# Optimization experiments

Measured on AMD Instinct MI355X. Metric: run time of the kernel, lower is better.

## Reference

```python
import jax, jax.numpy as jnp
import numpy as np

B, N, K = 16, 4096, 32

def setup_inputs() -> dict:
    key = jax.random.key(0)
    k0, k1, k2, k3, k4, k5 = jax.random.split(key, 6)
    frames_rot = jax.random.normal(k0, (B, N, 3, 3), jnp.float32)
    frames_trans = jax.random.normal(k1, (B, N, 3), jnp.float32)
    pair_rot = jax.random.normal(k2, (B, N, K, 3, 3), jnp.float32)
    pair_trans = jax.random.normal(k3, (B, N, K, 3), jnp.float32)
    confidences = jax.random.uniform(k4, (B, N, K, 1), jnp.float32)
    topology = jax.random.randint(k5, (B, N, K), 0, N, jnp.int32)
    return {"frames_rot": frames_rot, "frames_trans": frames_trans,
            "pair_rot": pair_rot, "pair_trans": pair_trans,
            "confidences": confidences, "topology": topology}


def _proj_with_svd(m):
    """Kabsch projection of batched [..., 3, 3] matrices onto SO(3) (det=+1)."""
    u, s, vh = jnp.linalg.svd(m, full_matrices=False)
    V = jnp.swapaxes(vh, -1, -2)
    d = jnp.sign(jnp.linalg.det(jnp.matmul(V, jnp.swapaxes(u, -1, -2))))  # [...]
    d3 = jnp.concatenate([jnp.ones(d.shape + (2,), m.dtype), d[..., None]], axis=-1)  # diag(1,1,d)
    # rot = V @ diag(1,1,d) @ u^T
    return jnp.einsum('...ik,...k,...jk->...ij', V, d3, u)


def reference(frames_rot, frames_trans, pair_rot, pair_trans, confidences, topology):
    # gather neighbor frames T_j: [B,N,K,3,3] / [B,N,K,3]
    gather = jax.vmap(lambda f, t: f[t])
    Tj_rot = gather(frames_rot, topology)
    Tj_trans = gather(frames_trans, topology)

    # normalized confidences p_ij over neighbors K
    w = jnp.squeeze(confidences, axis=-1)             # [B,N,K]
    p = w / jnp.sum(w, axis=2, keepdims=True)         # [B,N,K]

    # compose rigids: T_j * T_ji
    comp_rot = jnp.einsum('bnkij,bnkjl->bnkil', Tj_rot, pair_rot)                 # [B,N,K,3,3]
    comp_trans = jnp.einsum('bnkij,bnkj->bnki', Tj_rot, pair_trans) + Tj_trans    # [B,N,K,3]

    # confidence-weighted average over neighbors
    avg_rot = jnp.einsum('bnk,bnkij->bnij', p, comp_rot)    # [B,N,3,3]
    avg_trans = jnp.einsum('bnk,bnki->bni', p, comp_trans)  # [B,N,3]

    # project averaged rot onto SO(3), then invert (transpose) as in the module
    rot = _proj_with_svd(avg_rot)
    rot_inv = jnp.swapaxes(rot, -1, -2)                     # invert_rots of a rotation

    # pack (rot 9 + trans 3) -> [B,N,12]
    return jnp.concatenate([rot_inv.reshape(B, N, 9), avg_trans], axis=-1)
```

## Files before the change

kernel.cpp:

```cpp
#include <hip/hip_runtime.h>
#include <math.h>

#define N_RES 4096
#define KNB 32
#define BN_TOTAL 65536

typedef float v4f __attribute__((ext_vector_type(4)));
typedef int v4i __attribute__((ext_vector_type(4)));

template <int p, int q>
__device__ __forceinline__ void jacobi_rot(float S[3][3], float V[3][3]) {
    float apq = S[p][q];
    if (fabsf(apq) > 1e-20f) {
        float app = S[p][p], aqq = S[q][q];
        float tau = (aqq - app) / (2.0f * apq);
        float tt = (tau >= 0.0f ? 1.0f : -1.0f) / (fabsf(tau) + sqrtf(1.0f + tau * tau));
        float c = 1.0f / sqrtf(1.0f + tt * tt);
        float s = tt * c;
#pragma unroll
        for (int i = 0; i < 3; i++) {
            float Sip = S[i][p], Siq = S[i][q];
            S[i][p] = c * Sip - s * Siq;
            S[i][q] = s * Sip + c * Siq;
        }
#pragma unroll
        for (int i = 0; i < 3; i++) {
            float Spi = S[p][i], Sqi = S[q][i];
            S[p][i] = c * Spi - s * Sqi;
            S[q][i] = s * Spi + c * Sqi;
        }
#pragma unroll
        for (int i = 0; i < 3; i++) {
            float Vip = V[i][p], Viq = V[i][q];
            V[i][p] = c * Vip - s * Viq;
            V[i][q] = s * Vip + c * Viq;
        }
    }
}

template <int A, int Bc>
__device__ __forceinline__ void sort_pair(float lam[3], float V[3][3]) {
    if (lam[A] < lam[Bc]) {
        float tl = lam[A]; lam[A] = lam[Bc]; lam[Bc] = tl;
#pragma unroll
        for (int i = 0; i < 3; i++) {
            float tv = V[i][A]; V[i][A] = V[i][Bc]; V[i][Bc] = tv;
        }
    }
}

__device__ __forceinline__ void project_and_store(const float M[3][3],
                                                  float t0, float t1, float t2,
                                                  float* outp) {
    float S[3][3];
#pragma unroll
    for (int i = 0; i < 3; i++)
#pragma unroll
        for (int j = 0; j < 3; j++)
            S[i][j] = M[0][i] * M[0][j] + M[1][i] * M[1][j] + M[2][i] * M[2][j];
    float V[3][3] = {{1, 0, 0}, {0, 1, 0}, {0, 0, 1}};

#pragma unroll
    for (int sweep = 0; sweep < 4; sweep++) {
        jacobi_rot<0, 1>(S, V);
        jacobi_rot<0, 2>(S, V);
        jacobi_rot<1, 2>(S, V);
    }

    float lam[3] = {S[0][0], S[1][1], S[2][2]};
    sort_pair<0, 1>(lam, V);
    sort_pair<1, 2>(lam, V);
    sort_pair<0, 1>(lam, V);

    float detV = V[0][0] * (V[1][1] * V[2][2] - V[1][2] * V[2][1]) -
                 V[0][1] * (V[1][0] * V[2][2] - V[1][2] * V[2][0]) +
                 V[0][2] * (V[1][0] * V[2][1] - V[1][1] * V[2][0]);
    if (detV < 0.0f) { V[0][2] = -V[0][2]; V[1][2] = -V[1][2]; V[2][2] = -V[2][2]; }

    float Bm[3][3];
#pragma unroll
    for (int i = 0; i < 3; i++)
#pragma unroll
        for (int j = 0; j < 3; j++)
            Bm[i][j] = M[i][0] * V[0][j] + M[i][1] * V[1][j] + M[i][2] * V[2][j];

    float u0[3] = {Bm[0][0], Bm[1][0], Bm[2][0]};
    float n0 = u0[0] * u0[0] + u0[1] * u0[1] + u0[2] * u0[2];
    float rn0 = 1.0f / sqrtf(fmaxf(n0, 1e-24f));
    u0[0] *= rn0; u0[1] *= rn0; u0[2] *= rn0;

    float b1[3] = {Bm[0][1], Bm[1][1], Bm[2][1]};
    float d01 = u0[0] * b1[0] + u0[1] * b1[1] + u0[2] * b1[2];
    float u1[3] = {b1[0] - d01 * u0[0], b1[1] - d01 * u0[1], b1[2] - d01 * u0[2]};
    float n1 = u1[0] * u1[0] + u1[1] * u1[1] + u1[2] * u1[2];
    float rn1 = 1.0f / sqrtf(fmaxf(n1, 1e-24f));
    u1[0] *= rn1; u1[1] *= rn1; u1[2] *= rn1;

    float u2[3] = {u0[1] * u1[2] - u0[2] * u1[1],
                   u0[2] * u1[0] - u0[0] * u1[2],
                   u0[0] * u1[1] - u0[1] * u1[0]};

    float R[9];
#pragma unroll
    for (int i = 0; i < 3; i++) {
        float Ui0 = (i == 0 ? u0[0] : (i == 1 ? u0[1] : u0[2]));
        float Ui1 = (i == 0 ? u1[0] : (i == 1 ? u1[1] : u1[2]));
        float Ui2 = (i == 0 ? u2[0] : (i == 1 ? u2[1] : u2[2]));
#pragma unroll
        for (int j = 0; j < 3; j++)
            R[i * 3 + j] = Ui0 * V[j][0] + Ui1 * V[j][1] + Ui2 * V[j][2];
    }

    v4f* o4 = (v4f*)outp;
    o4[0] = (v4f){R[0], R[1], R[2], R[3]};
    o4[1] = (v4f){R[4], R[5], R[6], R[7]};
    o4[2] = (v4f){R[8], t0, t1, t2};
}

__global__ __launch_bounds__(256) void repack_kernel(
    const float* __restrict__ frames_rot,
    const float* __restrict__ frames_trans,
    float* __restrict__ pk)
{
    int row = blockIdx.x * 256 + threadIdx.x;
    const float* fr = frames_rot + (size_t)row * 9;
    const float* ft = frames_trans + (size_t)row * 3;
    v4f a = {fr[0], fr[1], fr[2], fr[3]};
    v4f b = {fr[4], fr[5], fr[6], fr[7]};
    v4f c = {fr[8], ft[0], ft[1], ft[2]};
    v4f* o = (v4f*)(pk + (size_t)row * 16);
    o[0] = a; o[1] = b; o[2] = c;
}

__global__ __launch_bounds__(256) void accum_kernel(
    const float* __restrict__ pk,
    const float* __restrict__ pair_rot,
    const float* __restrict__ pair_trans,
    const float* __restrict__ conf,
    const int* __restrict__ topo,
    float* __restrict__ acc)
{
    int tid = threadIdx.x;
    int bid = blockIdx.x;

    int xcd = bid & 7;
    int slot = bid >> 3;
    int batch = xcd + ((slot >> 7) << 3);
    int chunk = slot & 127;

    int elem = batch * N_RES + chunk * 32 + (tid >> 3);
    int t = tid & 7;

    size_t kbase = (size_t)elem * KNB + (size_t)t * 4;
    const v4f* pr4 = (const v4f*)(pair_rot + kbase * 9);
    const v4f* pt4 = (const v4f*)(pair_trans + kbase * 3);
    const v4f* cf4 = (const v4f*)(conf + kbase);
    const v4i* tp4 = (const v4i*)(topo + kbase);

    float prl[36];
#pragma unroll
    for (int i = 0; i < 9; i++) {
        v4f v = __builtin_nontemporal_load(pr4 + i);
        prl[4 * i + 0] = v.x; prl[4 * i + 1] = v.y;
        prl[4 * i + 2] = v.z; prl[4 * i + 3] = v.w;
    }
    float ptl[12];
#pragma unroll
    for (int i = 0; i < 3; i++) {
        v4f v = __builtin_nontemporal_load(pt4 + i);
        ptl[4 * i + 0] = v.x; ptl[4 * i + 1] = v.y;
        ptl[4 * i + 2] = v.z; ptl[4 * i + 3] = v.w;
    }
    v4f wv = __builtin_nontemporal_load(cf4);
    float wl[4] = {wv.x, wv.y, wv.z, wv.w};
    v4i jv = __builtin_nontemporal_load(tp4);
    int jl[4] = {jv.x, jv.y, jv.z, jv.w};

    float Macc[9] = {0, 0, 0, 0, 0, 0, 0, 0, 0};
    float tacc[3] = {0, 0, 0};
    float wsum = 0.0f;

    size_t pkbase = (size_t)batch * N_RES * 16;

#pragma unroll
    for (int kk = 0; kk < 4; kk++) {
        int j = jl[kk];
        const v4f* row = (const v4f*)(pk + pkbase + (size_t)j * 16);
        v4f fa = row[0], fb = row[1], fc = row[2];
        float r[9] = {fa.x, fa.y, fa.z, fa.w, fb.x, fb.y, fb.z, fb.w, fc.x};
        float tj[3] = {fc.y, fc.z, fc.w};

        float w = wl[kk];
        const float* pr = prl + kk * 9;
        const float* pt = ptl + kk * 3;
#pragma unroll
        for (int i = 0; i < 3; i++) {
#pragma unroll
            for (int l = 0; l < 3; l++) {
                float cij = r[i * 3 + 0] * pr[0 * 3 + l] +
                            r[i * 3 + 1] * pr[1 * 3 + l] +
                            r[i * 3 + 2] * pr[2 * 3 + l];
                Macc[i * 3 + l] += w * cij;
            }
            float ct = r[i * 3 + 0] * pt[0] + r[i * 3 + 1] * pt[1] +
                       r[i * 3 + 2] * pt[2] + tj[i];
            tacc[i] += w * ct;
        }
        wsum += w;
    }

#pragma unroll
    for (int st = 1; st <= 4; st <<= 1) {
#pragma unroll
        for (int i = 0; i < 9; i++) Macc[i] += __shfl_xor(Macc[i], st);
#pragma unroll
        for (int i = 0; i < 3; i++) tacc[i] += __shfl_xor(tacc[i], st);
        wsum += __shfl_xor(wsum, st);
    }

    if (t == 0) {
        v4f* o = (v4f*)(acc + (size_t)elem * 16);
        o[0] = (v4f){Macc[0], Macc[1], Macc[2], Macc[3]};
        o[1] = (v4f){Macc[4], Macc[5], Macc[6], Macc[7]};
        o[2] = (v4f){Macc[8], tacc[0], tacc[1], tacc[2]};
        o[3] = (v4f){wsum, 0.0f, 0.0f, 0.0f};
    }
}

__global__ __launch_bounds__(256) void solve_kernel(
    const float* __restrict__ acc,
    float* __restrict__ out)
{
    int elem = blockIdx.x * 256 + threadIdx.x;
    const v4f* a4 = (const v4f*)(acc + (size_t)elem * 16);
    v4f A0 = a4[0], A1 = a4[1], A2 = a4[2], A3 = a4[3];
    float inv_w = 1.0f / fmaxf(A3.x, 1e-20f);
    float M[3][3] = {{A0.x * inv_w, A0.y * inv_w, A0.z * inv_w},
                     {A0.w * inv_w, A1.x * inv_w, A1.y * inv_w},
                     {A1.z * inv_w, A1.w * inv_w, A2.x * inv_w}};
    float t0 = A2.y * inv_w, t1 = A2.z * inv_w, t2 = A2.w * inv_w;
    project_and_store(M, t0, t1, t2, out + (size_t)elem * 12);
}

__global__ __launch_bounds__(256) void fused_kernel(
    const float* __restrict__ frames_rot, const float* __restrict__ frames_trans,
    const float* __restrict__ pair_rot, const float* __restrict__ pair_trans,
    const float* __restrict__ conf, const int* __restrict__ topo,
    float* __restrict__ out)
{
    int tid = threadIdx.x;
    int bid = blockIdx.x;
    int xcd = bid & 7;
    int slot = bid >> 3;
    int batch = xcd + ((slot >> 7) << 3);
    int chunk = slot & 127;
    int elem = batch * N_RES + chunk * 32 + (tid >> 3);
    int t = tid & 7;

    const float* fr_b = frames_rot + (size_t)batch * N_RES * 9;
    const float* ft_b = frames_trans + (size_t)batch * N_RES * 3;

    size_t kbase = (size_t)elem * KNB + (size_t)t * 4;
    const v4f* pr4 = (const v4f*)(pair_rot + kbase * 9);
    const v4f* pt4 = (const v4f*)(pair_trans + kbase * 3);
    const v4f* cf4 = (const v4f*)(conf + kbase);
    const v4i* tp4 = (const v4i*)(topo + kbase);

    float prl[36];
#pragma unroll
    for (int i = 0; i < 9; i++) {
        v4f v = __builtin_nontemporal_load(pr4 + i);
        prl[4 * i] = v.x; prl[4 * i + 1] = v.y; prl[4 * i + 2] = v.z; prl[4 * i + 3] = v.w;
    }
    float ptl[12];
#pragma unroll
    for (int i = 0; i < 3; i++) {
        v4f v = __builtin_nontemporal_load(pt4 + i);
        ptl[4 * i] = v.x; ptl[4 * i + 1] = v.y; ptl[4 * i + 2] = v.z; ptl[4 * i + 3] = v.w;
    }
    v4f wv = __builtin_nontemporal_load(cf4);
    float wl[4] = {wv.x, wv.y, wv.z, wv.w};
    v4i jv = __builtin_nontemporal_load(tp4);
    int jl[4] = {jv.x, jv.y, jv.z, jv.w};

    float Macc[9] = {0, 0, 0, 0, 0, 0, 0, 0, 0};
    float tacc[3] = {0, 0, 0};
    float wsum = 0.0f;

#pragma unroll
    for (int kk = 0; kk < 4; kk++) {
        int j = jl[kk];
        const float* Rj = fr_b + j * 9;
        const float* Tj = ft_b + j * 3;
        float r[9];
#pragma unroll
        for (int i = 0; i < 9; i++) r[i] = Rj[i];
        float tj[3];
#pragma unroll
        for (int i = 0; i < 3; i++) tj[i] = Tj[i];
        float w = wl[kk];
        const float* pr = prl + kk * 9;
        const float* pt = ptl + kk * 3;
#pragma unroll
        for (int i = 0; i < 3; i++) {
#pragma unroll
            for (int l = 0; l < 3; l++) {
                float cij = r[i * 3] * pr[l] + r[i * 3 + 1] * pr[3 + l] + r[i * 3 + 2] * pr[6 + l];
                Macc[i * 3 + l] += w * cij;
            }
            float ct = r[i * 3] * pt[0] + r[i * 3 + 1] * pt[1] + r[i * 3 + 2] * pt[2] + tj[i];
            tacc[i] += w * ct;
        }
        wsum += w;
    }

#pragma unroll
    for (int st = 1; st <= 4; st <<= 1) {
#pragma unroll
        for (int i = 0; i < 9; i++) Macc[i] += __shfl_xor(Macc[i], st);
#pragma unroll
        for (int i = 0; i < 3; i++) tacc[i] += __shfl_xor(tacc[i], st);
        wsum += __shfl_xor(wsum, st);
    }

    float inv_w = 1.0f / fmaxf(wsum, 1e-20f);
    float M[3][3];
#pragma unroll
    for (int i = 0; i < 3; i++)
#pragma unroll
        for (int j = 0; j < 3; j++) M[i][j] = Macc[i * 3 + j] * inv_w;

    if (t == 0)
        project_and_store(M, tacc[0] * inv_w, tacc[1] * inv_w, tacc[2] * inv_w,
                          out + (size_t)elem * 12);
}

extern "C" void kernel_launch(void* const* d_in, const int* in_sizes, int n_in,
                              void* d_out, int out_size, void* d_ws, size_t ws_size,
                              hipStream_t stream) {
    const float* frames_rot = (const float*)d_in[0];
    const float* frames_trans = (const float*)d_in[1];
    const float* pair_rot = (const float*)d_in[2];
    const float* pair_trans = (const float*)d_in[3];
    const float* conf = (const float*)d_in[4];
    const int* topo = (const int*)d_in[5];
    float* out = (float*)d_out;

    const size_t PK_BYTES = (size_t)BN_TOTAL * 16 * sizeof(float);
    const size_t need = 2 * PK_BYTES;

    if (ws_size >= need) {
        float* pk = (float*)d_ws;
        float* acc = pk + (size_t)BN_TOTAL * 16;
        hipLaunchKernelGGL(repack_kernel, dim3(BN_TOTAL / 256), dim3(256), 0, stream,
                           frames_rot, frames_trans, pk);
        hipLaunchKernelGGL(accum_kernel, dim3(BN_TOTAL * 8 / 256), dim3(256), 0, stream,
                           pk, pair_rot, pair_trans, conf, topo, acc);
        hipLaunchKernelGGL(solve_kernel, dim3(BN_TOTAL / 256), dim3(256), 0, stream,
                           acc, out);
    } else {
        hipLaunchKernelGGL(fused_kernel, dim3(BN_TOTAL * 8 / 256), dim3(256), 0, stream,
                           frames_rot, frames_trans, pair_rot, pair_trans, conf, topo, out);
    }
}
```

Measured before the change: 202.5 us.

## Stage pair rotations through LDS and interleave neighbor assignment for coalescing

The accumulation kernel now stages each block's pair_rot data in shared memory in two halves using contiguous 16-byte loads spread across all threads. Threads then read their neighbors' rotations from LDS, and neighbors are assigned with stride 8 so that conf, topo and pair_trans loads coalesce across lanes. Gathers of neighbor frames are software-pipelined (two rows prefetched ahead), and occupancy is hinted with launch_bounds(256,8). This adds __syncthreads barriers and scalar loads for pair_trans, but aims to cut scattered per-thread 144-byte streaming reads.

```diff
diff --git a/kernel.cpp b/kernel.cpp
--- a/kernel.cpp
+++ b/kernel.cpp
@@ -132,7 +132,9 @@
     o[0] = a; o[1] = b; o[2] = c;
 }
 
-__global__ __launch_bounds__(256) void accum_kernel(
+#define LDS_E_STRIDE 148
+
+__global__ __launch_bounds__(256, 8) void accum_kernel(
     const float* __restrict__ pk,
     const float* __restrict__ pair_rot,
     const float* __restrict__ pair_trans,
@@ -140,73 +142,96 @@
     const int* __restrict__ topo,
     float* __restrict__ acc)
 {
+    __shared__ float lds_rot[32 * LDS_E_STRIDE];
+
     int tid = threadIdx.x;
     int bid = blockIdx.x;
 
     int xcd = bid & 7;
     int slot = bid >> 3;
     int batch = xcd + ((slot >> 7) << 3);
-    int chunk = slot & 127;
-
-    int elem = batch * N_RES + chunk * 32 + (tid >> 3);
+    int chunkidx = slot & 127;
+    int elem0 = batch * N_RES + chunkidx * 32;
+
+    int e = tid >> 3;
     int t = tid & 7;
-
-    size_t kbase = (size_t)elem * KNB + (size_t)t * 4;
-    const v4f* pr4 = (const v4f*)(pair_rot + kbase * 9);
-    const v4f* pt4 = (const v4f*)(pair_trans + kbase * 3);
-    const v4f* cf4 = (const v4f*)(conf + kbase);
-    const v4i* tp4 = (const v4i*)(topo + kbase);
-
-    float prl[36];
-#pragma unroll
-    for (int i = 0; i < 9; i++) {
-        v4f v = __builtin_nontemporal_load(pr4 + i);
-        prl[4 * i + 0] = v.x; prl[4 * i + 1] = v.y;
-        prl[4 * i + 2] = v.z; prl[4 * i + 3] = v.w;
-    }
+    int elem_g = elem0 + e;
+
+    float wl[4];
+    int jl[4];
     float ptl[12];
 #pragma unroll
-    for (int i = 0; i < 3; i++) {
-        v4f v = __builtin_nontemporal_load(pt4 + i);
-        ptl[4 * i + 0] = v.x; ptl[4 * i + 1] = v.y;
-        ptl[4 * i + 2] = v.z; ptl[4 * i + 3] = v.w;
-    }
-    v4f wv = __builtin_nontemporal_load(cf4);
-    float wl[4] = {wv.x, wv.y, wv.z, wv.w};
-    v4i jv = __builtin_nontemporal_load(tp4);
-    int jl[4] = {jv.x, jv.y, jv.z, jv.w};
+    for (int s = 0; s < 4; s++) {
+        size_t nidx = (size_t)elem_g * KNB + t + 8 * s;
+        wl[s] = __builtin_nontemporal_load(conf + nidx);
+        jl[s] = __builtin_nontemporal_load(topo + nidx);
+#pragma unroll
+        for (int c = 0; c < 3; c++)
+            ptl[s * 3 + c] = __builtin_nontemporal_load(pair_trans + nidx * 3 + c);
+    }
+
+    const float* pkb = pk + (size_t)batch * N_RES * 16;
+    v4f g0a, g0b, g0c, g1a, g1b, g1c;
+    {
+        const v4f* r0 = (const v4f*)(pkb + (size_t)jl[0] * 16);
+        const v4f* r1 = (const v4f*)(pkb + (size_t)jl[1] * 16);
+        g0a = r0[0]; g0b = r0[1]; g0c = r0[2];
+        g1a = r1[0]; g1b = r1[1]; g1c = r1[2];
+    }
 
     float Macc[9] = {0, 0, 0, 0, 0, 0, 0, 0, 0};
     float tacc[3] = {0, 0, 0};
-    float wsum = 0.0f;
-
-    size_t pkbase = (size_t)batch * N_RES * 16;
-
-#pragma unroll
-    for (int kk = 0; kk < 4; kk++) {
-        int j = jl[kk];
-        const v4f* row = (const v4f*)(pk + pkbase + (size_t)j * 16);
-        v4f fa = row[0], fb = row[1], fc = row[2];
-        float r[9] = {fa.x, fa.y, fa.z, fa.w, fb.x, fb.y, fb.z, fb.w, fc.x};
-        float tj[3] = {fc.y, fc.z, fc.w};
-
-        float w = wl[kk];
-        const float* pr = prl + kk * 9;
-        const float* pt = ptl + kk * 3;
-#pragma unroll
-        for (int i = 0; i < 3; i++) {
-#pragma unroll
-            for (int l = 0; l < 3; l++) {
-                float cij = r[i * 3 + 0] * pr[0 * 3 + l] +
-                            r[i * 3 + 1] * pr[1 * 3 + l] +
-                            r[i * 3 + 2] * pr[2 * 3 + l];
-                Macc[i * 3 + l] += w * cij;
+    float wsum = wl[0] + wl[1] + wl[2] + wl[3];
+
+#pragma unroll
+    for (int ch = 0; ch < 2; ch++) {
+        for (int i = tid; i < 1152; i += 256) {
+            int se = i / 36;
+            int r = i - se * 36;
+            const v4f* gp = (const v4f*)(pair_rot +
+                ((size_t)(elem0 + se) * KNB + ch * 16) * 9) + r;
+            v4f v = __builtin_nontemporal_load(gp);
+            *(v4f*)(lds_rot + se * LDS_E_STRIDE + r * 4) = v;
+        }
+        __syncthreads();
+
+#pragma unroll
+        for (int sc = 0; sc < 2; sc++) {
+            int s = 2 * ch + sc;
+            float w = wl[s];
+            const float* lp = lds_rot + e * LDS_E_STRIDE + 9 * (t + 8 * sc);
+            float pr[9];
+#pragma unroll
+            for (int c = 0; c < 9; c++) pr[c] = lp[c];
+
+            v4f fa = (s & 1) ? g1a : g0a;
+            v4f fb = (s & 1) ? g1b : g0b;
+            v4f fc = (s & 1) ? g1c : g0c;
+            float r[9] = {fa.x, fa.y, fa.z, fa.w, fb.x, fb.y, fb.z, fb.w, fc.x};
+            float tj[3] = {fc.y, fc.z, fc.w};
+            const float* pt = ptl + s * 3;
+
+#pragma unroll
+            for (int i = 0; i < 3; i++) {
+#pragma unroll
+                for (int l = 0; l < 3; l++) {
+                    float cij = r[i * 3 + 0] * pr[0 * 3 + l] +
+                                r[i * 3 + 1] * pr[1 * 3 + l] +
+                                r[i * 3 + 2] * pr[2 * 3 + l];
+                    Macc[i * 3 + l] += w * cij;
+                }
+                float ct = r[i * 3 + 0] * pt[0] + r[i * 3 + 1] * pt[1] +
+                           r[i * 3 + 2] * pt[2] + tj[i];
+                tacc[i] += w * ct;
             }
-            float ct = r[i * 3 + 0] * pt[0] + r[i * 3 + 1] * pt[1] +
-                       r[i * 3 + 2] * pt[2] + tj[i];
-            tacc[i] += w * ct;
-        }
-        wsum += w;
+
+            if (ch == 0) {
+                const v4f* rn = (const v4f*)(pkb + (size_t)jl[2 + sc] * 16);
+                if (sc == 0) { g0a = rn[0]; g0b = rn[1]; g0c = rn[2]; }
+                else         { g1a = rn[0]; g1b = rn[1]; g1c = rn[2]; }
+            }
+        }
+        if (ch == 0) __syncthreads();
     }
 
 #pragma unroll
@@ -219,7 +244,7 @@
     }
 
     if (t == 0) {
-        v4f* o = (v4f*)(acc + (size_t)elem * 16);
+        v4f* o = (v4f*)(acc + (size_t)elem_g * 16);
         o[0] = (v4f){Macc[0], Macc[1], Macc[2], Macc[3]};
         o[1] = (v4f){Macc[4], Macc[5], Macc[6], Macc[7]};
         o[2] = (v4f){Macc[8], tacc[0], tacc[1], tacc[2]};
@@ -354,7 +379,7 @@
         float* acc = pk + (size_t)BN_TOTAL * 16;
         hipLaunchKernelGGL(repack_kernel, dim3(BN_TOTAL / 256), dim3(256), 0, stream,
                            frames_rot, frames_trans, pk);
-        hipLaunchKernelGGL(accum_kernel, dim3(BN_TOTAL * 8 / 256), dim3(256), 0, stream,
+        hipLaunchKernelGGL(accum_kernel, dim3(BN_TOTAL / 32), dim3(256), 0, stream,
                            pk, pair_rot, pair_trans, conf, topo, acc);
         hipLaunchKernelGGL(solve_kernel, dim3(BN_TOTAL / 256), dim3(256), 0, stream,
                            acc, out);
```

After: 262.0 us. 29.4% more time.

## Stage pair data through LDS with one lane per neighbor in accum kernel

Applied to the files above, without the earlier changes.

The accumulation kernel now assigns one lane per neighbor (32 lanes per element, two elements per wave) instead of eight lanes each handling four neighbors. Pair rotations and translations are loaded as fully coalesced float4 streams into shared memory, then read back per lane. Each lane does a single gather of its neighbor frame, which exposes more independent gathers per wave. In exchange it adds an LDS round trip, a longer 5-step shuffle reduction, and more idle lanes on the final store.

```diff
diff --git a/kernel.cpp b/kernel.cpp
--- a/kernel.cpp
+++ b/kernel.cpp
@@ -125,11 +125,10 @@
     int row = blockIdx.x * 256 + threadIdx.x;
     const float* fr = frames_rot + (size_t)row * 9;
     const float* ft = frames_trans + (size_t)row * 3;
-    v4f a = {fr[0], fr[1], fr[2], fr[3]};
-    v4f b = {fr[4], fr[5], fr[6], fr[7]};
-    v4f c = {fr[8], ft[0], ft[1], ft[2]};
     v4f* o = (v4f*)(pk + (size_t)row * 16);
-    o[0] = a; o[1] = b; o[2] = c;
+    o[0] = (v4f){fr[0], fr[1], fr[2], fr[3]};
+    o[1] = (v4f){fr[4], fr[5], fr[6], fr[7]};
+    o[2] = (v4f){fr[8], ft[0], ft[1], ft[2]};
 }
 
 __global__ __launch_bounds__(256) void accum_kernel(
@@ -140,77 +139,69 @@
     const int* __restrict__ topo,
     float* __restrict__ acc)
 {
+    __shared__ float lds[4 * 768];
+
     int tid = threadIdx.x;
+    int wid = tid >> 6;
+    int L = tid & 63;
     int bid = blockIdx.x;
 
     int xcd = bid & 7;
     int slot = bid >> 3;
-    int batch = xcd + ((slot >> 7) << 3);
-    int chunk = slot & 127;
-
-    int elem = batch * N_RES + chunk * 32 + (tid >> 3);
-    int t = tid & 7;
-
-    size_t kbase = (size_t)elem * KNB + (size_t)t * 4;
-    const v4f* pr4 = (const v4f*)(pair_rot + kbase * 9);
-    const v4f* pt4 = (const v4f*)(pair_trans + kbase * 3);
-    const v4f* cf4 = (const v4f*)(conf + kbase);
-    const v4i* tp4 = (const v4i*)(topo + kbase);
-
-    float prl[36];
-#pragma unroll
-    for (int i = 0; i < 9; i++) {
-        v4f v = __builtin_nontemporal_load(pr4 + i);
-        prl[4 * i + 0] = v.x; prl[4 * i + 1] = v.y;
-        prl[4 * i + 2] = v.z; prl[4 * i + 3] = v.w;
-    }
-    float ptl[12];
+    int batch = xcd + ((slot >> 9) << 3);
+    int within = slot & 511;
+    int elem0 = batch * N_RES + within * 8 + wid * 2;
+
+    int h = L >> 5;
+    int k = L & 31;
+    int elem_g = elem0 + h;
+
+    float* wlds = lds + wid * 768;
+
+    size_t nidx = (size_t)elem0 * KNB + L;
+    float w = __builtin_nontemporal_load(conf + nidx);
+    int j = __builtin_nontemporal_load(topo + nidx);
+
+    const v4f* rg = (const v4f*)(pair_rot + (size_t)elem0 * (KNB * 9));
+    for (int s = L; s < 144; s += 64) {
+        v4f v = __builtin_nontemporal_load(rg + s);
+        *(v4f*)(wlds + 4 * s) = v;
+    }
+    const v4f* tg = (const v4f*)(pair_trans + (size_t)elem0 * (KNB * 3));
+    if (L < 48) {
+        v4f v = __builtin_nontemporal_load(tg + L);
+        *(v4f*)(wlds + 576 + 4 * L) = v;
+    }
+
+    const v4f* row = (const v4f*)(pk + ((size_t)batch * N_RES + (size_t)j) * 16);
+    v4f fa = row[0], fb = row[1], fc = row[2];
+    float r[9] = {fa.x, fa.y, fa.z, fa.w, fb.x, fb.y, fb.z, fb.w, fc.x};
+    float tj0 = fc.y, tj1 = fc.z, tj2 = fc.w;
+
+    const float* pr = wlds + h * 288 + k * 9;
+    float p[9];
+#pragma unroll
+    for (int c = 0; c < 9; c++) p[c] = pr[c];
+    const float* pt = wlds + 576 + h * 96 + k * 3;
+    float q0 = pt[0], q1 = pt[1], q2 = pt[2];
+
+    float Macc[9], tacc[3];
 #pragma unroll
     for (int i = 0; i < 3; i++) {
-        v4f v = __builtin_nontemporal_load(pt4 + i);
-        ptl[4 * i + 0] = v.x; ptl[4 * i + 1] = v.y;
-        ptl[4 * i + 2] = v.z; ptl[4 * i + 3] = v.w;
-    }
-    v4f wv = __builtin_nontemporal_load(cf4);
-    float wl[4] = {wv.x, wv.y, wv.z, wv.w};
-    v4i jv = __builtin_nontemporal_load(tp4);
-    int jl[4] = {jv.x, jv.y, jv.z, jv.w};
-
-    float Macc[9] = {0, 0, 0, 0, 0, 0, 0, 0, 0};
-    float tacc[3] = {0, 0, 0};
-    float wsum = 0.0f;
-
-    size_t pkbase = (size_t)batch * N_RES * 16;
-
-#pragma unroll
-    for (int kk = 0; kk < 4; kk++) {
-        int j = jl[kk];
-        const v4f* row = (const v4f*)(pk + pkbase + (size_t)j * 16);
-        v4f fa = row[0], fb = row[1], fc = row[2];
-        float r[9] = {fa.x, fa.y, fa.z, fa.w, fb.x, fb.y, fb.z, fb.w, fc.x};
-        float tj[3] = {fc.y, fc.z, fc.w};
-
-        float w = wl[kk];
-        const float* pr = prl + kk * 9;
-        const float* pt = ptl + kk * 3;
-#pragma unroll
-        for (int i = 0; i < 3; i++) {
-#pragma unroll
-            for (int l = 0; l < 3; l++) {
-                float cij = r[i * 3 + 0] * pr[0 * 3 + l] +
-                            r[i * 3 + 1] * pr[1 * 3 + l] +
-                            r[i * 3 + 2] * pr[2 * 3 + l];
-                Macc[i * 3 + l] += w * cij;
-            }
-            float ct = r[i * 3 + 0] * pt[0] + r[i * 3 + 1] * pt[1] +
-                       r[i * 3 + 2] * pt[2] + tj[i];
-            tacc[i] += w * ct;
-        }
-        wsum += w;
-    }
-
-#pragma unroll
-    for (int st = 1; st <= 4; st <<= 1) {
+#pragma unroll
+        for (int l = 0; l < 3; l++) {
+            Macc[i * 3 + l] = w * (r[i * 3 + 0] * p[0 * 3 + l] +
+                                   r[i * 3 + 1] * p[1 * 3 + l] +
+                                   r[i * 3 + 2] * p[2 * 3 + l]);
+        }
+        float tji = (i == 0 ? tj0 : (i == 1 ? tj1 : tj2));
+        tacc[i] = w * (r[i * 3 + 0] * q0 + r[i * 3 + 1] * q1 +
+                       r[i * 3 + 2] * q2 + tji);
+    }
+    float wsum = w;
+
+#pragma unroll
+    for (int st = 1; st <= 16; st <<= 1) {
 #pragma unroll
         for (int i = 0; i < 9; i++) Macc[i] += __shfl_xor(Macc[i], st);
 #pragma unroll
@@ -218,8 +209,8 @@
         wsum += __shfl_xor(wsum, st);
     }
 
-    if (t == 0) {
-        v4f* o = (v4f*)(acc + (size_t)elem * 16);
+    if (k == 0) {
+        v4f* o = (v4f*)(acc + (size_t)elem_g * 16);
         o[0] = (v4f){Macc[0], Macc[1], Macc[2], Macc[3]};
         o[1] = (v4f){Macc[4], Macc[5], Macc[6], Macc[7]};
         o[2] = (v4f){Macc[8], tacc[0], tacc[1], tacc[2]};
@@ -347,14 +338,15 @@
     float* out = (float*)d_out;
 
     const size_t PK_BYTES = (size_t)BN_TOTAL * 16 * sizeof(float);
-    const size_t need = 2 * PK_BYTES;
+    const size_t ACC_BYTES = (size_t)BN_TOTAL * 16 * sizeof(float);
+    const size_t need = PK_BYTES + ACC_BYTES;
 
     if (ws_size >= need) {
         float* pk = (float*)d_ws;
-        float* acc = pk + (size_t)BN_TOTAL * 16;
+        float* acc = (float*)((char*)d_ws + PK_BYTES);
         hipLaunchKernelGGL(repack_kernel, dim3(BN_TOTAL / 256), dim3(256), 0, stream,
                            frames_rot, frames_trans, pk);
-        hipLaunchKernelGGL(accum_kernel, dim3(BN_TOTAL * 8 / 256), dim3(256), 0, stream,
+        hipLaunchKernelGGL(accum_kernel, dim3(BN_TOTAL / 8), dim3(256), 0, stream,
                            pk, pair_rot, pair_trans, conf, topo, acc);
         hipLaunchKernelGGL(solve_kernel, dim3(BN_TOTAL / 256), dim3(256), 0, stream,
                            acc, out);
```

New measurement: 169.1 us, median of 2. -16.5%, faster.
